# Performance work log

Hardware: AMD Instinct MI355X
Metric: run time of the kernel (lower is better)

The kernel has to match this reference:

```python
import jax, jax.numpy as jnp
import numpy as np

N_NODES = 50000
N_EDGES = 400000
N_GRAPHS = 500
FEAT = 64
GNN_OUT = 32   # concat(src,dst) -> 64 == hardcoded input_dim
HID = 64
LABELS = 10


def _lin(key, fan_in, fan_out):
    kw, kb = jax.random.split(key)
    s = 1.0 / np.sqrt(fan_in)
    return (jax.random.uniform(kw, (fan_in, fan_out), jnp.float32, -s, s),
            jax.random.uniform(kb, (fan_out,), jnp.float32, -s, s))


def setup_inputs() -> dict:
    key = jax.random.key(0)
    ks = jax.random.split(key, 10)
    x = jax.random.normal(ks[0], (N_NODES, FEAT), jnp.float32)
    edge_index = jax.random.randint(ks[1], (2, N_EDGES), 0, N_NODES, jnp.int64 if jax.config.jax_enable_x64 else jnp.int32)
    state = jnp.zeros((N_EDGES,), jnp.bool_)           # no edges occupied yet
    batch = jnp.repeat(jnp.arange(N_GRAPHS), N_NODES // N_GRAPHS)  # 100 nodes/graph
    y = jax.random.randint(ks[2], (N_GRAPHS,), 0, LABELS)
    Wg, bg = _lin(ks[3], FEAT, GNN_OUT)
    W1, b1 = _lin(ks[4], 2 * GNN_OUT, HID * 4)
    W2, b2 = _lin(ks[5], HID * 4, HID * 2)
    W3, b3 = _lin(ks[6], HID * 2, HID)
    P1, pb1 = _lin(ks[7], HID, HID)
    P2, pb2 = _lin(ks[8], HID, LABELS)
    return {"x": x, "edge_index": edge_index, "state": state, "batch": batch, "y": y,
            "Wg": Wg, "bg": bg, "W1": W1, "b1": b1, "W2": W2, "b2": b2,
            "W3": W3, "b3": b3, "P1": P1, "pb1": pb1, "P2": P2, "pb2": pb2}


def reference(x, edge_index, state, batch, y, Wg, bg, W1, b1, W2, b2, W3, b3, P1, pb1, P2, pb2):
    n_nodes = x.shape[0]
    n_graphs = y.shape[0]
    n_edges = edge_index.shape[1]
    src, dst = edge_index[0], edge_index[1]

    def gnn_node_reps(emask):
        # one round of masked message passing: h_v = ELU((x_v + sum_{(u,v) in masked E} x_u) @ Wg + bg)
        msgs = x[src] * emask[:, None]                       # [E, F]
        agg = jax.ops.segment_sum(msgs, dst, num_segments=n_nodes)
        return jax.nn.elu((x + agg) @ Wg + bg)               # [N, 32]

    full_mask = jnp.ones((n_edges,), x.dtype)
    ocp_mask = state.astype(x.dtype)
    node_reps = gnn_node_reps(full_mask) - gnn_node_reps(ocp_mask)   # ava_node_reps

    # edge action reps: concat endpoint reps -> 64 -> MLP 256/128/64 with ELU
    reps = jnp.concatenate([node_reps[src], node_reps[dst]], axis=1)  # [E, 64]
    reps = jax.nn.elu(reps @ W1 + b1)
    reps = jax.nn.elu(reps @ W2 + b2)
    reps = reps @ W3 + b3                                             # [E, 64]

    # prob head + gather per-edge target label logit
    logits = jax.nn.elu(reps @ P1 + pb1) @ P2 + pb2                   # [E, L]
    abatch = batch[src]                                               # [E]
    lg = jnp.take_along_axis(logits, y[abatch][:, None], axis=1)[:, 0]

    # segment softmax over available edges within each graph (occupied -> -inf)
    avail = ~state
    lg = jnp.where(avail, lg, -jnp.inf)
    m = jax.ops.segment_max(lg, abatch, num_segments=n_graphs)
    ex = jnp.where(avail, jnp.exp(lg - m[abatch]), 0.0)
    denom = jax.ops.segment_sum(ex, abatch, num_segments=n_graphs)
    probs = ex / denom[abatch]                                        # [E]

    # scatter_max over probs per graph: value + first argmax edge id
    mp = jnp.where(avail, probs, -jnp.inf)
    added_action_probs = jax.ops.segment_max(mp, abatch, num_segments=n_graphs)
    cand = jnp.where(mp == added_action_probs[abatch], jnp.arange(n_edges), n_edges)
    added_actions = jax.ops.segment_min(cand, abatch, num_segments=n_graphs)
    return probs, added_action_probs, added_actions
```

## Files before the change

### kernel.cpp

```cpp
#include <hip/hip_runtime.h>
#include <math.h>

#define N_NODES   50000
#define N_EDGES   400000
#define N_GRAPHS  500
#define CAND_MAX  262144
#define DELTA     4e-3f
#define CAP       64

typedef __attribute__((ext_vector_type(8))) _Float16 f16x8;
typedef __attribute__((ext_vector_type(4))) float f32x4;

__device__ __forceinline__ float elu_f(float v) { return v > 0.f ? v : expm1f(v); }
__device__ __forceinline__ float elu_fast(float v) {
    return fmaxf(v, 0.f) + (__expf(fminf(v, 0.f)) - 1.f);
}
__device__ __forceinline__ unsigned enc_f(float f) {
    unsigned u = __float_as_uint(f);
    return (u & 0x80000000u) ? ~u : (u | 0x80000000u);
}
__device__ __forceinline__ float dec_f(unsigned u) {
    return __uint_as_float((u & 0x80000000u) ? (u & 0x7FFFFFFFu) : ~u);
}
__device__ __forceinline__ unsigned short f2h_bits(float f) {
    _Float16 h = (_Float16)f;
    return __builtin_bit_cast(unsigned short, h);
}
__device__ __forceinline__ float h2f(unsigned short b) {
    return (float)__builtin_bit_cast(_Float16, b);
}

__global__ void k_place(const int* __restrict__ src, const int* __restrict__ dst,
                        const unsigned char* __restrict__ state, const int* __restrict__ batch,
                        unsigned* __restrict__ cnt, unsigned* __restrict__ bucket,
                        unsigned short* __restrict__ meta,
                        const float* __restrict__ W1, const float* __restrict__ W2,
                        const float* __restrict__ W3, const float* __restrict__ P1,
                        const float* __restrict__ P2, char* __restrict__ Bpp,
                        float* __restrict__ Wt)
{
    if (blockIdx.x < 1563) {
        int e = blockIdx.x * 256 + threadIdx.x;
        if (e >= N_EDGES) return;
        int d = dst[e];
        int s = src[e];
        unsigned char st = state[e];
        unsigned idx = atomicAdd(&cnt[d], 1u);
        if (idx < CAP) bucket[d * CAP + idx] = (unsigned)s | (st ? 0x80000000u : 0u);
        int g = batch[s];
        meta[e] = (unsigned short)(g | (st ? 0 : 0x8000));
        return;
    }
    if (blockIdx.x >= 1624) {
        int t2 = (blockIdx.x - 1624) * 256 + threadIdx.x;
        if (t2 < 16384)      Wt[t2]         = W1[(t2 % 64) * 256 + t2 / 64];
        else if (t2 < 49152) { int t = t2 - 16384; Wt[t2] = W2[(t % 256) * 128 + t / 256]; }
        else if (t2 < 57344) { int t = t2 - 49152; Wt[t2] = W3[(t % 128) * 64 + t / 128]; }
        else                 { int t = t2 - 57344; Wt[t2] = P1[(t % 64) * 64 + t / 64]; }
        return;
    }
    int tid = (blockIdx.x - 1563) * 256 + threadIdx.x;
    if (tid >= 15616) return;
    const float* W; int K, NT, Nreal, base, i;
    if (tid < 4096)       { W = W1; K = 64;  NT = 16; Nreal = 256; base = 0;      i = tid; }
    else if (tid < 12288) { W = W2; K = 256; NT = 8;  Nreal = 128; base = 65536;  i = tid - 4096; }
    else if (tid < 14336) { W = W3; K = 128; NT = 4;  Nreal = 64;  base = 196608; i = tid - 12288; }
    else if (tid < 15360) { W = P1; K = 64;  NT = 4;  Nreal = 64;  base = 229376; i = tid - 14336; }
    else                  { W = P2; K = 64;  NT = 1;  Nreal = 10;  base = 245760; i = tid - 15360; }
    int KB = K / 32;
    int lane = i & 63; int i2 = i >> 6;
    int nt = i2 % NT; int i3 = i2 / NT;
    int kb = i3 % KB; int ps = i3 / KB;
    unsigned short s[8];
    #pragma unroll
    for (int j = 0; j < 8; ++j) {
        int k = kb * 32 + ((lane >> 4) << 3) + j;
        int n = nt * 16 + (lane & 15);
        float wv = (n < Nreal) ? W[k * Nreal + n] : 0.f;
        unsigned short h = f2h_bits(wv);
        s[j] = ps ? f2h_bits(wv - h2f(h)) : h;
    }
    uint4 u;
    u.x = (unsigned)s[0] | ((unsigned)s[1] << 16);
    u.y = (unsigned)s[2] | ((unsigned)s[3] << 16);
    u.z = (unsigned)s[4] | ((unsigned)s[5] << 16);
    u.w = (unsigned)s[6] | ((unsigned)s[7] << 16);
    int frag = (ps * KB + kb) * NT + nt;
    *reinterpret_cast<uint4*>(Bpp + base + frag * 1024 + lane * 16) = u;
}

__global__ void k_aggrep(const float* __restrict__ x, const unsigned* __restrict__ cnt,
                         const unsigned* __restrict__ bucket, const float* __restrict__ Wg,
                         const float* __restrict__ bg, float* __restrict__ reps)
{
    __shared__ float sv[4][128];
    const int w = threadIdx.x >> 6, j = threadIdx.x & 63;
    const int n = blockIdx.x * 4 + w;
    unsigned c = cnt[n]; if (c > CAP) c = CAP;
    float sf = 0.f, so = 0.f;
    for (unsigned i = 0; i < c; ++i) {
        unsigned p = bucket[n * CAP + i];
        float v = x[(p & 0x7FFFFFFFu) * 64 + j];
        sf += v;
        if (p & 0x80000000u) so += v;
    }
    float xv = x[n * 64 + j];
    sv[w][j]      = xv + sf;
    sv[w][64 + j] = xv + so;
    __syncthreads();
    const int o = j & 31;
    const float* svp = sv[w] + ((j >> 5) ? 64 : 0);
    float acc = 0.f;
    #pragma unroll 16
    for (int i = 0; i < 64; ++i) acc += svp[i] * Wg[i * 32 + o];
    float val = elu_fast(acc + bg[o]);
    float other = __shfl_xor(val, 32, 64);
    if (j < 32) reps[n * 32 + o] = val - other;
}

#define OFF_A 0
#define OFF_B 16384
#define SM_BYTES 49152

template<int K, int N, int ACT>
__device__ __forceinline__ void run_layer(char* sm, const char* gB, int inOff, int outOff,
                                          const float* __restrict__ bias, int w, int lane)
{
    constexpr int KB  = K / 32;
    constexpr int NT  = N / 16;
    constexpr int NTC = (NT < 8) ? NT : 8;
    constexpr int NH  = NT / NTC;
    constexpr int NTW = (NTC >= 4) ? (NTC / 4) : 1;

    __syncthreads();

    const int row0 = lane & 15;
    const int hi16 = (lane >> 4) * 16;

    #pragma unroll
    for (int nh = 0; nh < NH; ++nh) {
        f32x4 C[4][NTW];
        #pragma unroll
        for (int q = 0; q < NTW; ++q) {
            int nt = (w * NTW + q) % NTC;
            int n  = nh * NTC * 16 + nt * 16 + row0;
            float b = (ACT == 2) ? (n < 10 ? bias[n] : 0.f) : bias[n];
            #pragma unroll
            for (int mt = 0; mt < 4; ++mt) C[mt][q] = (f32x4){b, b, b, b};
        }

        #pragma unroll
        for (int kb = 0; kb < KB; ++kb) {
            f16x8 Ah[4];
            #pragma unroll
            for (int mt = 0; mt < 4; ++mt) {
                int row = mt * 16 + row0;
                int off = (((row * K + kb * 32) * 2) + hi16) ^ ((row & 7) << 4);
                Ah[mt] = *reinterpret_cast<const f16x8*>(sm + inOff + off);
            }
            #pragma unroll
            for (int q = 0; q < NTW; ++q) {
                int nt = (w * NTW + q) % NTC;
                const char* bp = gB + ((kb * NT + nh * NTC + nt) * 1024) + lane * 16;
                f16x8 Bh = *reinterpret_cast<const f16x8*>(bp);
                #pragma unroll
                for (int mt = 0; mt < 4; ++mt)
                    C[mt][q] = __builtin_amdgcn_mfma_f32_16x16x32_f16(Ah[mt], Bh, C[mt][q], 0, 0, 0);
                f16x8 Bl = *reinterpret_cast<const f16x8*>(bp + KB * NT * 1024);
                #pragma unroll
                for (int mt = 0; mt < 4; ++mt)
                    C[mt][q] = __builtin_amdgcn_mfma_f32_16x16x32_f16(Ah[mt], Bl, C[mt][q], 0, 0, 0);
            }
        }

        #pragma unroll
        for (int q = 0; q < NTW; ++q) {
            int nt = (w * NTW + q) % NTC;
            int n  = nh * NTC * 16 + nt * 16 + row0;
            #pragma unroll
            for (int mt = 0; mt < 4; ++mt) {
                #pragma unroll
                for (int r = 0; r < 4; ++r) {
                    int row = mt * 16 + (lane >> 4) * 4 + r;
                    float v = C[mt][q][r];
                    if (ACT == 1) v = elu_fast(v);
                    if (ACT == 2) {
                        *reinterpret_cast<float*>(sm + outOff + (row * 16 + n) * 4) = v;
                    } else {
                        int off = ((row * N + n) * 2) ^ ((row & 7) << 4);
                        *reinterpret_cast<unsigned short*>(sm + outOff + off) = f2h_bits(v);
                    }
                }
            }
        }
    }
}

__global__ __launch_bounds__(256, 3) void k_mlp(
    const float* __restrict__ reps, const int* __restrict__ src, const int* __restrict__ dst,
    const unsigned short* __restrict__ meta, const int* __restrict__ y,
    const float* __restrict__ b1, const float* __restrict__ b2, const float* __restrict__ b3,
    const float* __restrict__ pb1, const float* __restrict__ pb2,
    const char* __restrict__ Bpp, float* __restrict__ lg_out, unsigned* __restrict__ m_u)
{
    __shared__ char sm[SM_BYTES];
    __shared__ int sSrc[64], sDst[64], sG[64], sCol[64], sAvail[64];
    const int t = threadIdx.x, w = t >> 6, lane = t & 63;
    const int ebase = blockIdx.x * 64;

    if (t < 64) {
        int e = ebase + t;
        sSrc[t] = src[e]; sDst[t] = dst[e];
        unsigned m = meta[e];
        int g = m & 0x1ff;
        sG[t] = g; sCol[t] = y[g];
        sAvail[t] = (m >> 15) & 1;
    }
    __syncthreads();

    {
        int e = t >> 2, f0 = (t & 3) * 16;
        const float* rp = (f0 < 32) ? (reps + sSrc[e] * 32 + f0) : (reps + sDst[e] * 32 + (f0 - 32));
        float4 v0 = *reinterpret_cast<const float4*>(rp);
        float4 v1 = *reinterpret_cast<const float4*>(rp + 4);
        float4 v2 = *reinterpret_cast<const float4*>(rp + 8);
        float4 v3 = *reinterpret_cast<const float4*>(rp + 12);
        float vv[16] = {v0.x,v0.y,v0.z,v0.w, v1.x,v1.y,v1.z,v1.w,
                        v2.x,v2.y,v2.z,v2.w, v3.x,v3.y,v3.z,v3.w};
        unsigned pk[8];
        #pragma unroll
        for (int i = 0; i < 8; ++i)
            pk[i] = (unsigned)f2h_bits(vv[2*i]) | ((unsigned)f2h_bits(vv[2*i+1]) << 16);
        int b0 = (e * 64 + f0) * 2;
        uint4 u0 = {pk[0], pk[1], pk[2], pk[3]};
        uint4 u1 = {pk[4], pk[5], pk[6], pk[7]};
        *reinterpret_cast<uint4*>(sm + OFF_A + (b0 ^ ((e & 7) << 4)))        = u0;
        *reinterpret_cast<uint4*>(sm + OFF_A + ((b0 + 16) ^ ((e & 7) << 4))) = u1;
    }

    run_layer< 64, 256, 1>(sm, Bpp + 0,      OFF_A, OFF_B, b1,  w, lane);
    run_layer<256, 128, 1>(sm, Bpp + 65536,  OFF_B, OFF_A, b2,  w, lane);
    run_layer<128,  64, 0>(sm, Bpp + 196608, OFF_A, OFF_B, b3,  w, lane);
    run_layer< 64,  64, 1>(sm, Bpp + 229376, OFF_B, OFF_A, pb1, w, lane);
    run_layer< 64,  16, 2>(sm, Bpp + 245760, OFF_A, OFF_B, pb2, w, lane);
    __syncthreads();

    if (t < 64) {
        int col = sCol[t];
        float lg = *reinterpret_cast<const float*>(sm + OFF_B + (t * 16 + col) * 4);
        lg_out[ebase + t] = lg;
        float lgm = sAvail[t] ? lg : -INFINITY;
        atomicMax(&m_u[sG[t]], enc_f(lgm));
    }
}

__global__ void k_ex(const float* __restrict__ lg, const unsigned short* __restrict__ meta,
                     const unsigned* __restrict__ m_u, float* __restrict__ ex,
                     float* __restrict__ denom, unsigned* __restrict__ cand,
                     unsigned* __restrict__ ccnt)
{
    __shared__ float sden[N_GRAPHS];
    for (int i = threadIdx.x; i < N_GRAPHS; i += 256) sden[i] = 0.f;
    __syncthreads();
    for (int e = blockIdx.x * 256 + threadIdx.x; e < N_EDGES; e += gridDim.x * 256) {
        unsigned mt_ = meta[e];
        int g = mt_ & 0x1ff;
        float v = 0.f;
        if (mt_ & 0x8000) {
            float l = lg[e];
            float m = dec_f(m_u[g]);
            v = __expf(l - m);
            if (l >= m - DELTA) {
                unsigned i = atomicAdd(ccnt, 1u);
                if (i < CAND_MAX) cand[i] = (unsigned)e;
            }
        }
        ex[e] = v;
        atomicAdd(&sden[g], v);
    }
    __syncthreads();
    for (int i = threadIdx.x; i < N_GRAPHS; i += 256)
        if (sden[i] != 0.f) atomicAdd(&denom[i], sden[i]);
}

__global__ __launch_bounds__(256) void k_refine(
    const float* __restrict__ reps, const int* __restrict__ src, const int* __restrict__ dst,
    const unsigned short* __restrict__ meta, const int* __restrict__ y,
    const float* __restrict__ Wt,
    const float* __restrict__ b1, const float* __restrict__ b2, const float* __restrict__ b3,
    const float* __restrict__ pb1, const float* __restrict__ P2, const float* __restrict__ pb2,
    const float* __restrict__ ex, const float* __restrict__ denom, float* __restrict__ out,
    const unsigned* __restrict__ cand, const unsigned* __restrict__ ccnt,
    unsigned long long* __restrict__ key)
{
    for (int e = blockIdx.x * 256 + threadIdx.x; e < N_EDGES; e += gridDim.x * 256)
        out[e] = ex[e] / denom[meta[e] & 0x1ff];

    __shared__ float sa[4][256], sb[4][256];
    const int t = threadIdx.x, w = t >> 6, lane = t & 63;
    const float* W1t = Wt;
    const float* W2t = Wt + 16384;
    const float* W3t = Wt + 49152;
    const float* P1t = Wt + 57344;
    unsigned cnt = *ccnt; if (cnt > CAND_MAX) cnt = CAND_MAX;
    for (unsigned base = blockIdx.x * 4; base < cnt; base += gridDim.x * 4) {
        unsigned ci = base + w;
        bool act = ci < cnt;
        int g = 0, col = 0; unsigned e = 0;
        if (act) {
            e = cand[ci];
            int s_ = src[e], d_ = dst[e];
            g = meta[e] & 0x1ff; col = y[g];
            sa[w][lane] = (lane < 32) ? reps[s_ * 32 + lane] : reps[d_ * 32 + (lane - 32)];
        }
        __syncthreads();
        {
            float acc[4];
            #pragma unroll
            for (int r = 0; r < 4; ++r) acc[r] = b1[lane + 64 * r];
            #pragma unroll
            for (int k = 0; k < 64; k += 4) {
                float4 a = *reinterpret_cast<const float4*>(&sa[w][k]);
                #pragma unroll
                for (int r = 0; r < 4; ++r) {
                    float4 wv = *reinterpret_cast<const float4*>(&W1t[(lane + 64 * r) * 64 + k]);
                    acc[r] += a.x * wv.x + a.y * wv.y + a.z * wv.z + a.w * wv.w;
                }
            }
            #pragma unroll
            for (int r = 0; r < 4; ++r) sb[w][lane + 64 * r] = elu_f(acc[r]);
        }
        __syncthreads();
        {
            float acc0 = b2[lane], acc1 = b2[lane + 64];
            #pragma unroll
            for (int k = 0; k < 256; k += 4) {
                float4 a = *reinterpret_cast<const float4*>(&sb[w][k]);
                float4 w0 = *reinterpret_cast<const float4*>(&W2t[lane * 256 + k]);
                float4 w1 = *reinterpret_cast<const float4*>(&W2t[(lane + 64) * 256 + k]);
                acc0 += a.x * w0.x + a.y * w0.y + a.z * w0.z + a.w * w0.w;
                acc1 += a.x * w1.x + a.y * w1.y + a.z * w1.z + a.w * w1.w;
            }
            sa[w][lane] = elu_f(acc0); sa[w][lane + 64] = elu_f(acc1);
        }
        __syncthreads();
        {
            float acc = b3[lane];
            #pragma unroll
            for (int k = 0; k < 128; k += 4) {
                float4 a = *reinterpret_cast<const float4*>(&sa[w][k]);
                float4 wv = *reinterpret_cast<const float4*>(&W3t[lane * 128 + k]);
                acc += a.x * wv.x + a.y * wv.y + a.z * wv.z + a.w * wv.w;
            }
            sb[w][lane] = acc;
        }
        __syncthreads();
        float p1o;
        {
            float acc = pb1[lane];
            #pragma unroll
            for (int k = 0; k < 64; k += 4) {
                float4 a = *reinterpret_cast<const float4*>(&sb[w][k]);
                float4 wv = *reinterpret_cast<const float4*>(&P1t[lane * 64 + k]);
                acc += a.x * wv.x + a.y * wv.y + a.z * wv.z + a.w * wv.w;
            }
            p1o = elu_f(acc);
        }
        float part = act ? p1o * P2[lane * 10 + col] : 0.f;
        #pragma unroll
        for (int m = 32; m > 0; m >>= 1) part += __shfl_xor(part, m, 64);
        if (act && lane == 0) {
            float lgf = part + pb2[col];
            unsigned long long k64 = ((unsigned long long)enc_f(lgf) << 32) | (unsigned)(~e);
            atomicMax(&key[g], k64);
        }
        __syncthreads();
    }
}

__global__ void k_final(const float* __restrict__ denom, const unsigned long long* __restrict__ key,
                        float* __restrict__ out)
{
    int g = blockIdx.x * 256 + threadIdx.x;
    if (g >= N_GRAPHS) return;
    out[N_EDGES + g] = 1.0f / denom[g];
    unsigned long long k = key[g];
    out[N_EDGES + N_GRAPHS + g] = (float)(~(unsigned)(k & 0xFFFFFFFFull));
}

extern "C" void kernel_launch(void* const* d_in, const int* in_sizes, int n_in,
                              void* d_out, int out_size, void* d_ws, size_t ws_size,
                              hipStream_t stream)
{
    const float* x   = (const float*)d_in[0];
    const int*   ei  = (const int*)d_in[1];
    const int*   src = ei;
    const int*   dst = ei + N_EDGES;
    const unsigned char* state = (const unsigned char*)d_in[2];
    const int*   batch = (const int*)d_in[3];
    const int*   y     = (const int*)d_in[4];
    const float* Wg = (const float*)d_in[5];
    const float* bg = (const float*)d_in[6];
    const float* W1 = (const float*)d_in[7];
    const float* b1 = (const float*)d_in[8];
    const float* W2 = (const float*)d_in[9];
    const float* b2 = (const float*)d_in[10];
    const float* W3 = (const float*)d_in[11];
    const float* b3 = (const float*)d_in[12];
    const float* P1 = (const float*)d_in[13];
    const float* pb1= (const float*)d_in[14];
    const float* P2 = (const float*)d_in[15];
    const float* pb2= (const float*)d_in[16];

    float* ws = (float*)d_ws;
    unsigned*           bucket = (unsigned*)ws;
    unsigned*           cnt    = (unsigned*)(ws + 3200000);
    unsigned*           m_u    = (unsigned*)(ws + 3250000);
    float*              denom  = (float*)(ws + 3250500);
    unsigned*           ccnt   = (unsigned*)(ws + 3251000);
    unsigned long long* key    = (unsigned long long*)(ws + 3251002);
    float*              reps   = ws + 3252004;
    float*              lg     = ws + 4852004;
    float*              ex     = ws + 5252004;
    unsigned short*     meta   = (unsigned short*)(ws + 5652004);
    char*               Bpp    = (char*)(ws + 5852004);
    unsigned*           cand   = (unsigned*)(ws + 5914468);
    float*              Wt     = ws + 6176612;

    hipMemsetAsync(cnt, 0, (size_t)(3252002 - 3200000) * 4, stream);

    k_place  <<<1864, 256, 0, stream>>>(src, dst, state, batch, cnt, bucket, meta,
                                        W1, W2, W3, P1, P2, Bpp, Wt);
    k_aggrep <<<N_NODES / 4, 256, 0, stream>>>(x, cnt, bucket, Wg, bg, reps);
    k_mlp    <<<N_EDGES / 64, 256, 0, stream>>>(reps, src, dst, meta, y,
                                                b1, b2, b3, pb1, pb2, Bpp, lg, m_u);
    k_ex     <<<256, 256, 0, stream>>>(lg, meta, m_u, ex, denom, cand, ccnt);
    k_refine <<<1024, 256, 0, stream>>>(reps, src, dst, meta, y, Wt,
                                        b1, b2, b3, pb1, P2, pb2,
                                        ex, denom, (float*)d_out,
                                        cand, ccnt, key);
    k_final  <<<2, 256, 0, stream>>>(denom, key, (float*)d_out);
}
```

Baseline: 374.4 us.

## Split first MLP layer into halves to shrink LDS and raise occupancy

The first two MLP layers are now interleaved: layer 1 is computed in two 128-column halves, and each half is consumed right away as a partial K-slice of layer 2, accumulating into register accumulators. This means the 256-wide intermediate never has to live in shared memory, so the LDS footprint drops from 48KB to 32KB and launch bounds move from 3 to 4 blocks per CU. Separately, Wg is pre-transposed in the setup kernel so that the node aggregation kernel can read weights with float4 vector loads. The cost is extra barriers and more accumulator registers held across phases, which could put the 4-block occupancy target under register pressure.

```diff
diff --git a/kernel.cpp b/kernel.cpp
--- a/kernel.cpp
+++ b/kernel.cpp
@@ -34,6 +34,7 @@
                         const unsigned char* __restrict__ state, const int* __restrict__ batch,
                         unsigned* __restrict__ cnt, unsigned* __restrict__ bucket,
                         unsigned short* __restrict__ meta,
+                        const float* __restrict__ Wg,
                         const float* __restrict__ W1, const float* __restrict__ W2,
                         const float* __restrict__ W3, const float* __restrict__ P1,
                         const float* __restrict__ P2, char* __restrict__ Bpp,
@@ -56,7 +57,8 @@
         if (t2 < 16384)      Wt[t2]         = W1[(t2 % 64) * 256 + t2 / 64];
         else if (t2 < 49152) { int t = t2 - 16384; Wt[t2] = W2[(t % 256) * 128 + t / 256]; }
         else if (t2 < 57344) { int t = t2 - 49152; Wt[t2] = W3[(t % 128) * 64 + t / 128]; }
-        else                 { int t = t2 - 57344; Wt[t2] = P1[(t % 64) * 64 + t / 64]; }
+        else if (t2 < 61440) { int t = t2 - 57344; Wt[t2] = P1[(t % 64) * 64 + t / 64]; }
+        else if (t2 < 63488) { int t = t2 - 61440; Wt[t2] = Wg[(t % 64) * 32 + t / 64]; }
         return;
     }
     int tid = (blockIdx.x - 1563) * 256 + threadIdx.x;
@@ -90,7 +92,7 @@
 }
 
 __global__ void k_aggrep(const float* __restrict__ x, const unsigned* __restrict__ cnt,
-                         const unsigned* __restrict__ bucket, const float* __restrict__ Wg,
+                         const unsigned* __restrict__ bucket, const float* __restrict__ Wgt,
                          const float* __restrict__ bg, float* __restrict__ reps)
 {
     __shared__ float sv[4][128];
@@ -110,9 +112,17 @@
     __syncthreads();
     const int o = j & 31;
     const float* svp = sv[w] + ((j >> 5) ? 64 : 0);
+    const float* wp  = Wgt + o * 64;
     float acc = 0.f;
-    #pragma unroll 16
-    for (int i = 0; i < 64; ++i) acc += svp[i] * Wg[i * 32 + o];
+    #pragma unroll
+    for (int i = 0; i < 64; i += 4) {
+        float4 a = *reinterpret_cast<const float4*>(svp + i);
+        float4 b = *reinterpret_cast<const float4*>(wp + i);
+        acc += a.x * b.x;
+        acc += a.y * b.y;
+        acc += a.z * b.z;
+        acc += a.w * b.w;
+    }
     float val = elu_fast(acc + bg[o]);
     float other = __shfl_xor(val, 32, 64);
     if (j < 32) reps[n * 32 + o] = val - other;
@@ -120,7 +130,7 @@
 
 #define OFF_A 0
 #define OFF_B 16384
-#define SM_BYTES 49152
+#define SM_BYTES 32768
 
 template<int K, int N, int ACT>
 __device__ __forceinline__ void run_layer(char* sm, const char* gB, int inOff, int outOff,
@@ -196,7 +206,92 @@
     }
 }
 
-__global__ __launch_bounds__(256, 3) void k_mlp(
+template<int H>
+__device__ __forceinline__ void l1_half(char* sm, const char* gB, const float* __restrict__ b1,
+                                        int w, int lane)
+{
+    const int row0 = lane & 15;
+    const int hi16 = (lane >> 4) * 16;
+    f32x4 C[4][2];
+    #pragma unroll
+    for (int q = 0; q < 2; ++q) {
+        int nt = (w * 2 + q) & 7;
+        float b = b1[H * 128 + nt * 16 + row0];
+        #pragma unroll
+        for (int mt = 0; mt < 4; ++mt) C[mt][q] = (f32x4){b, b, b, b};
+    }
+    #pragma unroll
+    for (int kb = 0; kb < 2; ++kb) {
+        f16x8 Ah[4];
+        #pragma unroll
+        for (int mt = 0; mt < 4; ++mt) {
+            int row = mt * 16 + row0;
+            int off = (((row * 64 + kb * 32) * 2) + hi16) ^ ((row & 7) << 4);
+            Ah[mt] = *reinterpret_cast<const f16x8*>(sm + OFF_A + off);
+        }
+        #pragma unroll
+        for (int q = 0; q < 2; ++q) {
+            int nt = (w * 2 + q) & 7;
+            const char* bp = gB + ((kb * 16 + H * 8 + nt) * 1024) + lane * 16;
+            f16x8 Bh = *reinterpret_cast<const f16x8*>(bp);
+            #pragma unroll
+            for (int mt = 0; mt < 4; ++mt)
+                C[mt][q] = __builtin_amdgcn_mfma_f32_16x16x32_f16(Ah[mt], Bh, C[mt][q], 0, 0, 0);
+            f16x8 Bl = *reinterpret_cast<const f16x8*>(bp + 32768);
+            #pragma unroll
+            for (int mt = 0; mt < 4; ++mt)
+                C[mt][q] = __builtin_amdgcn_mfma_f32_16x16x32_f16(Ah[mt], Bl, C[mt][q], 0, 0, 0);
+        }
+    }
+    #pragma unroll
+    for (int q = 0; q < 2; ++q) {
+        int nt = (w * 2 + q) & 7;
+        int nl = nt * 16 + row0;
+        #pragma unroll
+        for (int mt = 0; mt < 4; ++mt) {
+            #pragma unroll
+            for (int r = 0; r < 4; ++r) {
+                int row = mt * 16 + (lane >> 4) * 4 + r;
+                float v = elu_fast(C[mt][q][r]);
+                int off = ((row * 128 + nl) * 2) ^ ((row & 7) << 4);
+                *reinterpret_cast<unsigned short*>(sm + OFF_B + off) = f2h_bits(v);
+            }
+        }
+    }
+}
+
+template<int H>
+__device__ __forceinline__ void l2_partial(char* sm, const char* gB, f32x4 (&C2)[4][2],
+                                           int w, int lane)
+{
+    const int row0 = lane & 15;
+    const int hi16 = (lane >> 4) * 16;
+    #pragma unroll
+    for (int kbl = 0; kbl < 4; ++kbl) {
+        f16x8 Ah[4];
+        #pragma unroll
+        for (int mt = 0; mt < 4; ++mt) {
+            int row = mt * 16 + row0;
+            int off = (((row * 128 + kbl * 32) * 2) + hi16) ^ ((row & 7) << 4);
+            Ah[mt] = *reinterpret_cast<const f16x8*>(sm + OFF_B + off);
+        }
+        #pragma unroll
+        for (int q = 0; q < 2; ++q) {
+            int nt = (w * 2 + q) & 7;
+            const char* bp = gB + (((H * 4 + kbl) * 8 + nt) * 1024) + lane * 16;
+            f16x8 Bh = *reinterpret_cast<const f16x8*>(bp);
+            #pragma unroll
+            for (int mt = 0; mt < 4; ++mt)
+                C2[mt][q] = __builtin_amdgcn_mfma_f32_16x16x32_f16(Ah[mt], Bh, C2[mt][q], 0, 0, 0);
+            f16x8 Bl = *reinterpret_cast<const f16x8*>(bp + 65536);
+            #pragma unroll
+            for (int mt = 0; mt < 4; ++mt)
+                C2[mt][q] = __builtin_amdgcn_mfma_f32_16x16x32_f16(Ah[mt], Bl, C2[mt][q], 0, 0, 0);
+        }
+    }
+}
+
+__global__ __launch_bounds__(256, 4) void k_mlp(
     const float* __restrict__ reps, const int* __restrict__ src, const int* __restrict__ dst,
     const unsigned short* __restrict__ meta, const int* __restrict__ y,
     const float* __restrict__ b1, const float* __restrict__ b2, const float* __restrict__ b3,
@@ -237,9 +332,43 @@
         *reinterpret_cast<uint4*>(sm + OFF_A + (b0 ^ ((e & 7) << 4)))        = u0;
         *reinterpret_cast<uint4*>(sm + OFF_A + ((b0 + 16) ^ ((e & 7) << 4))) = u1;
     }
-
-    run_layer< 64, 256, 1>(sm, Bpp + 0,      OFF_A, OFF_B, b1,  w, lane);
-    run_layer<256, 128, 1>(sm, Bpp + 65536,  OFF_B, OFF_A, b2,  w, lane);
+    __syncthreads();
+
+    l1_half<0>(sm, Bpp, b1, w, lane);
+    __syncthreads();
+
+    const int row0 = lane & 15;
+    f32x4 C2[4][2];
+    #pragma unroll
+    for (int q = 0; q < 2; ++q) {
+        int nt = (w * 2 + q) & 7;
+        float b = b2[nt * 16 + row0];
+        #pragma unroll
+        for (int mt = 0; mt < 4; ++mt) C2[mt][q] = (f32x4){b, b, b, b};
+    }
+    l2_partial<0>(sm, Bpp + 65536, C2, w, lane);
+    __syncthreads();
+
+    l1_half<1>(sm, Bpp, b1, w, lane);
+    __syncthreads();
+
+    l2_partial<1>(sm, Bpp + 65536, C2, w, lane);
+    #pragma unroll
+    for (int q = 0; q < 2; ++q) {
+        int nt = (w * 2 + q) & 7;
+        int nl = nt * 16 + row0;
+        #pragma unroll
+        for (int mt = 0; mt < 4; ++mt) {
+            #pragma unroll
+            for (int r = 0; r < 4; ++r) {
+                int row = mt * 16 + (lane >> 4) * 4 + r;
+                float v = elu_fast(C2[mt][q][r]);
+                int off = ((row * 128 + nl) * 2) ^ ((row & 7) << 4);
+                *reinterpret_cast<unsigned short*>(sm + OFF_A + off) = f2h_bits(v);
+            }
+        }
+    }
+
     run_layer<128,  64, 0>(sm, Bpp + 196608, OFF_A, OFF_B, b3,  w, lane);
     run_layer< 64,  64, 1>(sm, Bpp + 229376, OFF_B, OFF_A, pb1, w, lane);
     run_layer< 64,  16, 2>(sm, Bpp + 245760, OFF_A, OFF_B, pb2, w, lane);
@@ -426,12 +555,13 @@
     char*               Bpp    = (char*)(ws + 5852004);
     unsigned*           cand   = (unsigned*)(ws + 5914468);
     float*              Wt     = ws + 6176612;
+    float*              Wgt    = Wt + 61440;
 
     hipMemsetAsync(cnt, 0, (size_t)(3252002 - 3200000) * 4, stream);
 
-    k_place  <<<1864, 256, 0, stream>>>(src, dst, state, batch, cnt, bucket, meta,
-                                        W1, W2, W3, P1, P2, Bpp, Wt);
-    k_aggrep <<<N_NODES / 4, 256, 0, stream>>>(x, cnt, bucket, Wg, bg, reps);
+    k_place  <<<1872, 256, 0, stream>>>(src, dst, state, batch, cnt, bucket, meta,
+                                        Wg, W1, W2, W3, P1, P2, Bpp, Wt);
+    k_aggrep <<<N_NODES / 4, 256, 0, stream>>>(x, cnt, bucket, Wgt, bg, reps);
     k_mlp    <<<N_EDGES / 64, 256, 0, stream>>>(reps, src, dst, meta, y,
                                                 b1, b2, b3, pb1, pb2, Bpp, lg, m_u);
     k_ex     <<<256, 256, 0, stream>>>(lg, meta, m_u, ex, denom, cand, ccnt);
```

After: 562.6 us. 1.5x slower.
